# Optimization experiments

Measured on AMD Instinct MI355X. Metric: run time of the kernel, lower is better.

## Reference

```python
import jax, jax.numpy as jnp
import numpy as np

# SLAYER neuron / simulation parameters (from netParams)
THETA = 10.0      # spike threshold
TAU_SR = 10.0     # synaptic (psp) alpha-kernel time constant
TAU_REF = 1.0     # refractory alpha-kernel time constant
SCALE_REF = 2.0   # refractory kernel scale
TS = 1.0          # simulation time step

N, C, H, W_SP, T = 8, 2, 50, 63, 500
OUT = 128


def _alpha_scan(x_t_first, tau, gain):
    """Causal convolution with alpha kernel k[dt] = gain*(dt*TS/tau)*exp(1-dt*TS/tau),
    k[0]=0, expressed as an exact 2-state linear recursion (O(T) instead of O(T^2)).
    x_t_first: [T, ...]. Returns [T, ...]."""
    r = jnp.exp(jnp.asarray(-TS / tau, x_t_first.dtype))
    c = jnp.asarray(gain * (TS / tau) * np.e, x_t_first.dtype)

    def step(carry, xt):
        A, B = carry          # A = sum c*dt*r^dt, B = sum c*r^dt over past inputs
        out = A               # kernel is 0 at dt=0, so x[t] does not contribute yet
        Bp = B + c * xt
        return (r * (A + Bp), r * Bp), out

    zeros = jnp.zeros_like(x_t_first[0])
    _, out = jax.lax.scan(step, (zeros, zeros), x_t_first)
    return out


def _spike_scan(u_t_first):
    """SLAYER getSpikes: sequential threshold with refractory alpha kernel
    nu[dt] = -SCALE_REF*THETA*(dt*TS/TAU_REF)*exp(1-dt*TS/TAU_REF).
    u_t_first: [T, N, O] membrane input. Returns spikes [T, N, O]."""
    r = jnp.exp(jnp.asarray(-TS / TAU_REF, u_t_first.dtype))
    c = jnp.asarray(-SCALE_REF * THETA * (TS / TAU_REF) * np.e, u_t_first.dtype)

    def step(carry, ut):
        A, B = carry
        u = ut + A                       # membrane + accumulated refractory response
        s = (u >= THETA).astype(u.dtype)
        Bp = B + c * s
        return (r * (A + Bp), r * Bp), s

    zeros = jnp.zeros_like(u_t_first[0])
    _, s = jax.lax.scan(step, (zeros, zeros), u_t_first)
    return s


def setup_inputs() -> dict:
    key = jax.random.key(0)
    k1, k2 = jax.random.split(key)
    downsampled = (jax.random.uniform(k1, (N, C, H, W_SP, T)) < 0.05).astype(jnp.float32)
    W = jax.random.normal(k2, (OUT, C * H * W_SP), dtype=jnp.float32) * 0.05
    return {"downsampled": downsampled, "W": W}


def reference(downsampled, W):
    # psp: alpha-kernel temporal filter over every input element
    x = jnp.moveaxis(downsampled, -1, 0)            # [T, N, C, H, W]
    a = _alpha_scan(x, TAU_SR, 1.0)                  # [T, N, C, H, W]
    # dense: full-spatial projection per time step
    a = a.reshape(T, N, C * H * W_SP)                # [T, N, CHW]
    u = jnp.einsum('tnc,oc->tno', a, W)              # [T, N, OUT]
    # spike generation with refractory dynamics
    s = _spike_scan(u)                               # [T, N, OUT]
    s = jnp.moveaxis(s, 0, -1)                       # [N, OUT, T]
    return s.reshape(N, OUT, 1, 1, T)                # SLAYER dense output layout
```

## Files before the change

### kernel.cpp

```cpp
#include <hip/hip_runtime.h>

#define NB 8
#define CHW 6300
#define TT 500
#define OUT 128
#define NO 1024
#define NK32 200
#define KSPLIT 8
#define NKC (NK32/KSPLIT)

typedef __attribute__((ext_vector_type(8))) _Float16 f16x8;
typedef __attribute__((ext_vector_type(4))) float f32x4;

__device__ __forceinline__ void wg_barrier_lgkm() {
    asm volatile("s_waitcnt lgkmcnt(0)" ::: "memory");
    __builtin_amdgcn_s_barrier();
}

__global__ __launch_bounds__(256, 2) void gemm(const float* __restrict__ x,
                                               const float* __restrict__ W,
                                               float* __restrict__ vp) {
    const int L = blockIdx.x;
    const int logical = (L & 7) * 64 + (L >> 3);
    const int tb = logical & 7;
    const int n  = (logical >> 3) & 7;
    const int ks = logical >> 6;

    const int tid = threadIdx.x;
    const int wave = tid >> 6;
    const int lane = tid & 63;
    const int l15 = lane & 15;
    const int lg  = lane >> 4;
    const int rr  = lg;
    const int ch  = l15;
    const int k32_0 = ks * NKC;

    __shared__ float    Ls[2][32][65];
    __shared__ _Float16 Bs[2][4][512];

    const float* xn = x + (size_t)n * CHW * TT;
    const int toff = tb * 64 + ch * 4;
    const bool tbok = (tb < 7);

    f32x4 acc[2][4][2] = {};
    f16x8 Ar0[2][2], Ar1[2][2];
    float4 sA[2], sB[2];
    const float4 f4z = make_float4(0.f, 0.f, 0.f, 0.f);

#define XG(set, it)                                                                \
    {                                                                              \
        _Pragma("unroll") for (int p_ = 0; p_ < 2; p_++) {                         \
            const int r_ = wave * 8 + p_ * 4 + rr;                                 \
            const int c_ = (k32_0 + (it)) * 32 + r_;                               \
            const bool v_ = (c_ < CHW) && (tbok || ch < 13);                       \
            set[p_] = v_ ? *(const float4*)(xn + (size_t)c_ * TT + toff) : f4z;    \
        }                                                                          \
    }

#define DSW(set, bufL)                                                             \
    {                                                                              \
        _Pragma("unroll") for (int p_ = 0; p_ < 2; p_++) {                         \
            const int r_ = wave * 8 + p_ * 4 + rr;                                 \
            Ls[bufL][r_][ch * 4 + 0] = set[p_].x;                                  \
            Ls[bufL][r_][ch * 4 + 1] = set[p_].y;                                  \
            Ls[bufL][r_][ch * 4 + 2] = set[p_].z;                                  \
            Ls[bufL][r_][ch * 4 + 3] = set[p_].w;                                  \
        }                                                                          \
    }

#define TRANS(bufL, bufB)                                                          \
    {                                                                              \
        float tv_[8];                                                              \
        _Pragma("unroll") for (int i = 0; i < 8; i++)                              \
            tv_[i] = Ls[bufL][lg * 8 + i][wave * 16 + l15];                        \
        union { _Float16 h[8]; uint4 u; } tc_;                                     \
        _Pragma("unroll") for (int i = 0; i < 8; i++)                              \
            tc_.h[i] = (_Float16)tv_[i];                                           \
        *(uint4*)&Bs[bufB][wave][lane * 8] = tc_.u;                                \
    }

#define WLOAD(Ar, it)                                                              \
    {                                                                              \
        const int c_ = (k32_0 + (it)) * 32 + lg * 8;                               \
        _Pragma("unroll") for (int of = 0; of < 2; of++) {                         \
            const int o_ = (wave * 2 + of) * 16 + l15;                             \
            const float* wp_ = W + (size_t)o_ * CHW + c_;                          \
            float wv_[8];                                                          \
            if (c_ + 8 <= CHW) {                                                   \
                float4 a_ = *(const float4*)(wp_);                                 \
                float4 b_ = *(const float4*)(wp_ + 4);                             \
                wv_[0] = a_.x; wv_[1] = a_.y; wv_[2] = a_.z; wv_[3] = a_.w;        \
                wv_[4] = b_.x; wv_[5] = b_.y; wv_[6] = b_.z; wv_[7] = b_.w;        \
            } else {                                                               \
                _Pragma("unroll") for (int i = 0; i < 8; i++)                      \
                    wv_[i] = (c_ + i < CHW) ? wp_[i] : 0.f;                        \
            }                                                                      \
            union { _Float16 h[8]; f16x8 v; } hi_, lo_;                            \
            _Pragma("unroll") for (int i = 0; i < 8; i++) {                        \
                _Float16 h_ = (_Float16)wv_[i];                                    \
                hi_.h[i] = h_;                                                     \
                lo_.h[i] = (_Float16)((wv_[i] - (float)h_) * 2048.f);              \
            }                                                                      \
            Ar[of][0] = hi_.v;                                                     \
            Ar[of][1] = lo_.v;                                                     \
        }                                                                          \
    }

#define COMPUTE(buf, Ar)                                                           \
    {                                                                              \
        f16x8 bfr[4];                                                              \
        _Pragma("unroll") for (int tf = 0; tf < 4; tf++)                           \
            bfr[tf] = *(const f16x8*)&Bs[buf][tf][lane * 8];                       \
        _Pragma("unroll") for (int of = 0; of < 2; of++)                           \
            _Pragma("unroll") for (int tf = 0; tf < 4; tf++)                       \
                _Pragma("unroll") for (int hl = 0; hl < 2; hl++)                   \
                    acc[of][tf][hl] = __builtin_amdgcn_mfma_f32_16x16x32_f16(      \
                        Ar[of][hl], bfr[tf], acc[of][tf][hl], 0, 0, 0);            \
    }

    XG(sA, 0)
    XG(sB, 1)
    DSW(sA, 0)
    XG(sA, 2)
    wg_barrier_lgkm();
    TRANS(0, 0)
    DSW(sB, 1)
    XG(sB, 3)
    WLOAD(Ar0, 0)
    wg_barrier_lgkm();

    for (int p = 0; p < 12; ++p) {
        const int it = 2 * p;
        WLOAD(Ar1, it + 1)
        DSW(sA, 0)
        if (p <= 10) { XG(sA, it + 4) }
        TRANS(1, 1)
        COMPUTE(0, Ar0)
        wg_barrier_lgkm();
        WLOAD(Ar0, it + 2)
        if (p <= 10) { DSW(sB, 1) }
        if (p <= 9)  { XG(sB, it + 5) }
        TRANS(0, 0)
        COMPUTE(1, Ar1)
        wg_barrier_lgkm();
    }
    COMPUTE(0, Ar0)

    const float inv = 1.f / 2048.f;
#pragma unroll
    for (int of = 0; of < 2; of++) {
        const int o0 = (wave * 2 + of) * 16 + lg * 4;
#pragma unroll
        for (int tf = 0; tf < 4; tf++) {
            const int t = tb * 64 + tf * 16 + l15;
            if (t < TT) {
                f32x4 vo;
#pragma unroll
                for (int r = 0; r < 4; r++)
                    vo[r] = acc[of][tf][0][r] + acc[of][tf][1][r] * inv;
                *(f32x4*)(vp + (((size_t)ks * TT + t) * NB + n) * OUT + o0) = vo;
            }
        }
    }
#undef XG
#undef DSW
#undef TRANS
#undef WLOAD
#undef COMPUTE
}

#define SCN_RA 0.9048374180359595f
#define SCN_RACA 0.24596031111569496f
#define SCN_RS 0.36787944117144233f
#define SCN_RSCS -20.0f
#define SCN_RSCS2 -40.0f
#define SCN_RSRSCS -7.3575888234288467f
#define SCN_TH 10.0f

#define CHAIN_STEP(i)                                                   \
    {                                                                   \
        float ua = Aa;                                                  \
        float w = fmaf(SCN_RS, G, ua);                                  \
        float u = sp ? (w + SCN_RSCS) : w;                              \
        bool sn = (u >= SCN_TH);                                        \
        sbuf[i][lane] = sn ? 1.f : 0.f;                                 \
        float Gb = fmaf(SCN_RS, G, H);                                  \
        G = sp ? (Gb + SCN_RSCS2) : Gb;                                 \
        float Hb = SCN_RS * H;                                          \
        H = sp ? (Hb + SCN_RSRSCS) : Hb;                                \
        sp = sn;                                                        \
        Ba = fmaf(SCN_RA, Ba, SCN_RACA * vv[i]);                        \
        Aa = fmaf(SCN_RA, Aa, Ba);                                      \
    }

__global__ __launch_bounds__(512) void scanspike(const float* __restrict__ vp,
                                                 float* __restrict__ out) {
    const int tid = threadIdx.x;
    const int wave = tid >> 6;
    const int lane = tid & 63;
    const int l5 = lane & 31;
    const int rh = lane >> 5;
    const int g0 = blockIdx.x * 32;
    const int cn = g0 >> 7;
    const int co = (g0 & 127) + l5;

    __shared__ float vbuf[2][64][32];
    __shared__ float sbuf[64][33];

    for (int rp = wave; rp * 2 < 64; rp += 8) {
        int r = rp * 2 + rh;
        float a = 0.f;
#pragma unroll
        for (int k = 0; k < KSPLIT; k++)
            a += vp[(((size_t)k * TT + r) * NB + cn) * OUT + co];
        vbuf[0][r][l5] = a;
    }
    __syncthreads();

    float Aa = 0.f, Ba = 0.f, G = 0.f, H = 0.f;
    bool sp = false;

    for (int tb = 0; tb < 8; ++tb) {
        const int cur = tb & 1;
        const int t0 = tb * 64;
        const int cnt = (tb == 7) ? 52 : 64;

        if (wave == 0) {
            if (lane < 32) {
                if (cnt == 64) {
                    float vv[64];
#pragma unroll
                    for (int i = 0; i < 64; ++i) vv[i] = vbuf[cur][i][l5];
#pragma unroll
                    for (int i = 0; i < 64; ++i) CHAIN_STEP(i)
                } else {
                    float vv[52];
#pragma unroll
                    for (int i = 0; i < 52; ++i) vv[i] = vbuf[cur][i][l5];
#pragma unroll
                    for (int i = 0; i < 52; ++i) CHAIN_STEP(i)
                }
            }
        } else if (tb < 7) {
            const int nt0 = t0 + 64;
            const int ncnt = (tb == 6) ? 52 : 64;
            for (int rp = wave - 1; rp * 2 < ncnt; rp += 7) {
                int r = rp * 2 + rh;
                float a = 0.f;
#pragma unroll
                for (int k = 0; k < KSPLIT; k++)
                    a += vp[(((size_t)k * TT + nt0 + r) * NB + cn) * OUT + co];
                vbuf[cur ^ 1][r][l5] = a;
            }
        }
        __syncthreads();

#pragma unroll
        for (int j = 0; j < 4; ++j) {
            int cc = wave * 4 + j;
            int oo = (g0 & 127) + cc;
            if (lane < cnt)
                out[((size_t)cn * OUT + oo) * TT + t0 + lane] = sbuf[lane][cc];
        }
        __syncthreads();
    }
}

extern "C" void kernel_launch(void* const* d_in, const int* in_sizes, int n_in,
                              void* d_out, int out_size, void* d_ws, size_t ws_size,
                              hipStream_t stream) {
    const float* x = (const float*)d_in[0];
    const float* W = (const float*)d_in[1];
    float* out = (float*)d_out;

    float* vp = (float*)d_ws;

    gemm<<<512, 256, 0, stream>>>(x, W, vp);
    scanspike<<<32, 512, 0, stream>>>(vp, out);
}
```

Measured before the change: 62.46 us.

## Prepack W into split fp16 MFMA layout and restructure GEMM tiling per wave

Adds a packW kernel that converts W once per call into hi/lo fp16 fragments already laid out for the MFMA A operand, so the GEMM no longer converts or splits W inside its loop. The GEMM is retiled so each wave owns a 16-timestep slice for all 128 outputs and transposes its own x tile through a small per-wave LDS buffer. W chunks for several k-steps are staged into shared LDS and reused by all four waves. This adds an extra kernel launch and a workspace round trip for the packed weights, and changes the memory access pattern for x.

```diff
diff --git a/kernel.cpp b/kernel.cpp
--- a/kernel.cpp
+++ b/kernel.cpp
@@ -8,6 +8,7 @@
 #define NK32 200
 #define KSPLIT 8
 #define NKC (NK32/KSPLIT)
+#define CK 4
 
 typedef __attribute__((ext_vector_type(8))) _Float16 f16x8;
 typedef __attribute__((ext_vector_type(4))) float f32x4;
@@ -17,156 +18,154 @@
     __builtin_amdgcn_s_barrier();
 }
 
+__global__ __launch_bounds__(512) void packW(const float* __restrict__ W,
+                                             _Float16* __restrict__ Wp) {
+    const int tid = threadIdx.x;
+    const int of = tid >> 6;
+    const int lane = tid & 63;
+    const int k32 = blockIdx.x;
+    const int hl = blockIdx.y;
+    const int o = of * 16 + (lane & 15);
+    const int cb = k32 * 32 + (lane >> 4) * 8;
+
+    union { _Float16 h[8]; uint4 u; } tmp;
+#pragma unroll
+    for (int i = 0; i < 8; i++) {
+        int c = cb + i;
+        float w = (c < CHW) ? W[(size_t)o * CHW + c] : 0.f;
+        _Float16 hi = (_Float16)w;
+        tmp.h[i] = (hl == 0) ? hi : (_Float16)((w - (float)hi) * 2048.f);
+    }
+    size_t lr = (((size_t)hl * NK32 + k32) * 8 + of) * 64 + lane;
+    *(uint4*)(Wp + lr * 8) = tmp.u;
+}
+
 __global__ __launch_bounds__(256, 2) void gemm(const float* __restrict__ x,
-                                               const float* __restrict__ W,
+                                               const _Float16* __restrict__ Wp,
                                                float* __restrict__ vp) {
     const int L = blockIdx.x;
-    const int logical = (L & 7) * 64 + (L >> 3);
-    const int tb = logical & 7;
-    const int n  = (logical >> 3) & 7;
-    const int ks = logical >> 6;
-
+    const int ks = L & 7;
+    const int TG = L >> 3;
     const int tid = threadIdx.x;
-    const int wave = tid >> 6;
+    const int w = tid >> 6;
     const int lane = tid & 63;
     const int l15 = lane & 15;
-    const int lg  = lane >> 4;
-    const int rr  = lg;
-    const int ch  = l15;
+    const int lg = lane >> 4;
+    const int T = TG * 4 + w;
+    const int n = T >> 5;
+    const int t0 = (T & 31) * 16;
     const int k32_0 = ks * NKC;
 
-    __shared__ float    Ls[2][32][65];
-    __shared__ _Float16 Bs[2][4][512];
+    __shared__ __align__(16) _Float16 Wl[CK][16][512];
+    __shared__ float Xl[4][32][17];
 
     const float* xn = x + (size_t)n * CHW * TT;
-    const int toff = tb * 64 + ch * 4;
-    const bool tbok = (tb < 7);
-
-    f32x4 acc[2][4][2] = {};
-    f16x8 Ar0[2][2], Ar1[2][2];
-    float4 sA[2], sB[2];
+    const int xr = lane >> 2;
+    const int xc4 = (lane & 3) * 4;
+    const bool t_ok = (t0 + xc4 + 4) <= TT;
     const float4 f4z = make_float4(0.f, 0.f, 0.f, 0.f);
 
-#define XG(set, it)                                                                \
-    {                                                                              \
-        _Pragma("unroll") for (int p_ = 0; p_ < 2; p_++) {                         \
-            const int r_ = wave * 8 + p_ * 4 + rr;                                 \
-            const int c_ = (k32_0 + (it)) * 32 + r_;                               \
-            const bool v_ = (c_ < CHW) && (tbok || ch < 13);                       \
-            set[p_] = v_ ? *(const float4*)(xn + (size_t)c_ * TT + toff) : f4z;    \
-        }                                                                          \
-    }
-
-#define DSW(set, bufL)                                                             \
-    {                                                                              \
-        _Pragma("unroll") for (int p_ = 0; p_ < 2; p_++) {                         \
-            const int r_ = wave * 8 + p_ * 4 + rr;                                 \
-            Ls[bufL][r_][ch * 4 + 0] = set[p_].x;                                  \
-            Ls[bufL][r_][ch * 4 + 1] = set[p_].y;                                  \
-            Ls[bufL][r_][ch * 4 + 2] = set[p_].z;                                  \
-            Ls[bufL][r_][ch * 4 + 3] = set[p_].w;                                  \
-        }                                                                          \
-    }
-
-#define TRANS(bufL, bufB)                                                          \
-    {                                                                              \
-        float tv_[8];                                                              \
-        _Pragma("unroll") for (int i = 0; i < 8; i++)                              \
-            tv_[i] = Ls[bufL][lg * 8 + i][wave * 16 + l15];                        \
-        union { _Float16 h[8]; uint4 u; } tc_;                                     \
-        _Pragma("unroll") for (int i = 0; i < 8; i++)                              \
-            tc_.h[i] = (_Float16)tv_[i];                                           \
-        *(uint4*)&Bs[bufB][wave][lane * 8] = tc_.u;                                \
-    }
-
-#define WLOAD(Ar, it)                                                              \
-    {                                                                              \
-        const int c_ = (k32_0 + (it)) * 32 + lg * 8;                               \
-        _Pragma("unroll") for (int of = 0; of < 2; of++) {                         \
-            const int o_ = (wave * 2 + of) * 16 + l15;                             \
-            const float* wp_ = W + (size_t)o_ * CHW + c_;                          \
-            float wv_[8];                                                          \
-            if (c_ + 8 <= CHW) {                                                   \
-                float4 a_ = *(const float4*)(wp_);                                 \
-                float4 b_ = *(const float4*)(wp_ + 4);                             \
-                wv_[0] = a_.x; wv_[1] = a_.y; wv_[2] = a_.z; wv_[3] = a_.w;        \
-                wv_[4] = b_.x; wv_[5] = b_.y; wv_[6] = b_.z; wv_[7] = b_.w;        \
-            } else {                                                               \
-                _Pragma("unroll") for (int i = 0; i < 8; i++)                      \
-                    wv_[i] = (c_ + i < CHW) ? wp_[i] : 0.f;                        \
-            }                                                                      \
-            union { _Float16 h[8]; f16x8 v; } hi_, lo_;                            \
-            _Pragma("unroll") for (int i = 0; i < 8; i++) {                        \
-                _Float16 h_ = (_Float16)wv_[i];                                    \
-                hi_.h[i] = h_;                                                     \
-                lo_.h[i] = (_Float16)((wv_[i] - (float)h_) * 2048.f);              \
-            }                                                                      \
-            Ar[of][0] = hi_.v;                                                     \
-            Ar[of][1] = lo_.v;                                                     \
-        }                                                                          \
-    }
-
-#define COMPUTE(buf, Ar)                                                           \
-    {                                                                              \
-        f16x8 bfr[4];                                                              \
-        _Pragma("unroll") for (int tf = 0; tf < 4; tf++)                           \
-            bfr[tf] = *(const f16x8*)&Bs[buf][tf][lane * 8];                       \
-        _Pragma("unroll") for (int of = 0; of < 2; of++)                           \
-            _Pragma("unroll") for (int tf = 0; tf < 4; tf++)                       \
-                _Pragma("unroll") for (int hl = 0; hl < 2; hl++)                   \
-                    acc[of][tf][hl] = __builtin_amdgcn_mfma_f32_16x16x32_f16(      \
-                        Ar[of][hl], bfr[tf], acc[of][tf][hl], 0, 0, 0);            \
-    }
-
-    XG(sA, 0)
-    XG(sB, 1)
-    DSW(sA, 0)
-    XG(sA, 2)
-    wg_barrier_lgkm();
-    TRANS(0, 0)
-    DSW(sB, 1)
-    XG(sB, 3)
-    WLOAD(Ar0, 0)
-    wg_barrier_lgkm();
-
-    for (int p = 0; p < 12; ++p) {
-        const int it = 2 * p;
-        WLOAD(Ar1, it + 1)
-        DSW(sA, 0)
-        if (p <= 10) { XG(sA, it + 4) }
-        TRANS(1, 1)
-        COMPUTE(0, Ar0)
+    f32x4 acc[8][2] = {};
+    float4 q0[2], q1[2], q2[2], q3[2];
+
+#define XG(qq, it_)                                                            \
+    {                                                                          \
+        _Pragma("unroll") for (int p_ = 0; p_ < 2; p_++) {                     \
+            const int c_ = (k32_0 + (it_)) * 32 + xr + 16 * p_;                \
+            qq[p_] = (c_ < CHW && t_ok)                                        \
+                ? *(const float4*)(xn + (size_t)c_ * TT + t0 + xc4)            \
+                : f4z;                                                         \
+        }                                                                      \
+    }
+
+#define DSW(qq)                                                                \
+    {                                                                          \
+        _Pragma("unroll") for (int p_ = 0; p_ < 2; p_++) {                     \
+            const int r_ = xr + 16 * p_;                                       \
+            Xl[w][r_][xc4 + 0] = qq[p_].x;                                     \
+            Xl[w][r_][xc4 + 1] = qq[p_].y;                                     \
+            Xl[w][r_][xc4 + 2] = qq[p_].z;                                     \
+            Xl[w][r_][xc4 + 3] = qq[p_].w;                                     \
+        }                                                                      \
+    }
+
+#define TRANS(bfr_)                                                            \
+    {                                                                          \
+        union { _Float16 h[8]; f16x8 v; } tc_;                                 \
+        _Pragma("unroll") for (int i_ = 0; i_ < 8; i_++)                       \
+            tc_.h[i_] = (_Float16)Xl[w][lg * 8 + i_][l15];                     \
+        bfr_ = tc_.v;                                                          \
+    }
+
+#define STEPCOMP(kk_, bfr_)                                                    \
+    {                                                                          \
+        _Pragma("unroll") for (int of_ = 0; of_ < 8; of_++)                    \
+            _Pragma("unroll") for (int hl_ = 0; hl_ < 2; hl_++) {              \
+                f16x8 a_ = *(const f16x8*)&Wl[kk_][of_ * 2 + hl_][lane * 8];   \
+                acc[of_][hl_] = __builtin_amdgcn_mfma_f32_16x16x32_f16(        \
+                    a_, bfr_, acc[of_][hl_], 0, 0, 0);                         \
+            }                                                                  \
+    }
+
+#define STEP(kk_, qcur_, qnext_)                                               \
+    {                                                                          \
+        f16x8 bfr_;                                                            \
+        TRANS(bfr_)                                                            \
+        if (c0 + (kk_) + 1 < NKC) { DSW(qnext_) }                              \
+        if (c0 + (kk_) + 4 < NKC) { XG(qcur_, c0 + (kk_) + 4) }                \
+        STEPCOMP(kk_, bfr_)                                                    \
+    }
+
+    XG(q0, 0)
+    XG(q1, 1)
+    XG(q2, 2)
+    XG(q3, 3)
+    DSW(q0)
+
+    for (int ck = 0; ck < 7; ++ck) {
+        const int c0 = ck * CK;
+        const int csz = (c0 + CK <= NKC) ? CK : (NKC - c0);
+
         wg_barrier_lgkm();
-        WLOAD(Ar0, it + 2)
-        if (p <= 10) { DSW(sB, 1) }
-        if (p <= 9)  { XG(sB, it + 5) }
-        TRANS(0, 0)
-        COMPUTE(1, Ar1)
+        for (int i_ = 0; i_ < csz * 4; ++i_) {
+            int f_ = i_ * 4 + (tid >> 6);
+            int kk_ = f_ >> 4, ofhl_ = f_ & 15;
+            int of_ = ofhl_ >> 1, hl_ = ofhl_ & 1;
+            int k32_ = k32_0 + c0 + kk_;
+            uint4 v_ = *(const uint4*)(Wp +
+                ((((size_t)hl_ * NK32 + k32_) * 8 + of_) * 64 + lane) * 8);
+            *(uint4*)&Wl[kk_][ofhl_][lane * 8] = v_;
+        }
         wg_barrier_lgkm();
-    }
-    COMPUTE(0, Ar0)
+
+        if (csz == CK) {
+            STEP(0, q0, q1)
+            STEP(1, q1, q2)
+            STEP(2, q2, q3)
+            STEP(3, q3, q0)
+        } else {
+            STEP(0, q0, q1)
+        }
+    }
 
     const float inv = 1.f / 2048.f;
-#pragma unroll
-    for (int of = 0; of < 2; of++) {
-        const int o0 = (wave * 2 + of) * 16 + lg * 4;
-#pragma unroll
-        for (int tf = 0; tf < 4; tf++) {
-            const int t = tb * 64 + tf * 16 + l15;
-            if (t < TT) {
-                f32x4 vo;
-#pragma unroll
-                for (int r = 0; r < 4; r++)
-                    vo[r] = acc[of][tf][0][r] + acc[of][tf][1][r] * inv;
-                *(f32x4*)(vp + (((size_t)ks * TT + t) * NB + n) * OUT + o0) = vo;
-            }
+    const int t = t0 + l15;
+    if (t < TT) {
+#pragma unroll
+        for (int of = 0; of < 8; of++) {
+            f32x4 vo;
+#pragma unroll
+            for (int r = 0; r < 4; r++)
+                vo[r] = acc[of][0][r] + acc[of][1][r] * inv;
+            *(f32x4*)(vp + (((size_t)ks * TT + t) * NB + n) * OUT +
+                      of * 16 + lg * 4) = vo;
         }
     }
 #undef XG
 #undef DSW
 #undef TRANS
-#undef WLOAD
-#undef COMPUTE
+#undef STEPCOMP
+#undef STEP
 }
 
 #define SCN_RA 0.9048374180359595f
@@ -273,8 +272,10 @@
     const float* W = (const float*)d_in[1];
     float* out = (float*)d_out;
 
-    float* vp = (float*)d_ws;
-
-    gemm<<<512, 256, 0, stream>>>(x, W, vp);
+    _Float16* Wp = (_Float16*)d_ws;
+    float*    vp = (float*)((char*)d_ws + 3276800);
+
+    packW<<<dim3(NK32, 2), 512, 0, stream>>>(W, Wp);
+    gemm<<<512, 256, 0, stream>>>(x, Wp, vp);
     scanspike<<<32, 512, 0, stream>>>(vp, out);
 }
```

After: 73.55 us. 1.18x slower.
